# Optimization experiments

Measured on AMD Instinct MI355X. Metric: run time of the kernel, lower is better.

The kernel has to match this reference:

```python
import jax, jax.numpy as jnp
import numpy as np

B, N, E, G, V = 8, 512, 8192, 1024, 100000
HD, FIN, BN_EPS = 1024, 20, 1e-5


def setup_inputs() -> dict:
    key = jax.random.key(0)
    ks = jax.random.split(key, 8)
    return {
        'h': jax.random.normal(ks[0], (B, N, FIN), jnp.float32),
        'src': jax.random.randint(ks[1], (B, E), 0, N, jnp.int32),
        'dst': jax.random.randint(ks[2], (B, E), 0, N, jnp.int32),
        'gPos': jax.random.randint(ks[3], (B, G), 0, V, jnp.int32),
        'allDBGEmb': jax.random.normal(ks[4], (V, HD), jnp.float32),
        'fc_init_w': jax.random.normal(ks[5], (HD, FIN), jnp.float32) * (1.0 / np.sqrt(FIN)),
        'fc_init_b': jnp.zeros((HD,), jnp.float32),
        'bn1_g': jnp.ones((HD,), jnp.float32),
        'bn1_b': jnp.zeros((HD,), jnp.float32),
        'bn2_g': jnp.ones((HD,), jnp.float32),
        'bn2_b': jnp.zeros((HD,), jnp.float32),
        'fc_w': jax.random.normal(ks[6], (128, 2 * HD), jnp.float32) * (1.0 / np.sqrt(2 * HD)),
        'fc_b': jnp.zeros((128,), jnp.float32),
        'bn3_g': jnp.ones((128,), jnp.float32),
        'bn3_b': jnp.zeros((128,), jnp.float32),
        'fc2_w': jax.random.normal(ks[7], (1, 128), jnp.float32) * (1.0 / np.sqrt(128)),
        'fc2_b': jnp.zeros((1,), jnp.float32),
    }


def _bn(x, g, b):
    # BatchNorm1d in training mode: batch statistics over axis 0 (biased var)
    mu = x.mean(0)
    var = ((x - mu) ** 2).mean(0)
    return (x - mu) * jax.lax.rsqrt(var + BN_EPS) * g + b


def _gin_mean(x, s, d):
    # GINConv(None, 'mean') with eps=0: h_v + mean_{u in N(v)} h_u
    sums = jax.ops.segment_sum(x[s], d, num_segments=N)  # [N, HD]
    deg = jax.ops.segment_sum(jnp.ones((E, 1), x.dtype), d, num_segments=N)
    return x + jnp.where(deg > 0, sums / jnp.maximum(deg, 1.0), 0.0)


def reference(h, src, dst, gPos, allDBGEmb, fc_init_w, fc_init_b,
              bn1_g, bn1_b, bn2_g, bn2_b, fc_w, fc_b, bn3_g, bn3_b,
              fc2_w, fc2_b):
    def per_graph(hq, s, d, gp):
        x = hq @ fc_init_w.T + fc_init_b                      # [N, HD]
        x = jax.nn.relu(_bn(_gin_mean(x, s, d), bn1_g, bn1_b))
        x = jax.nn.relu(_bn(_gin_mean(x, s, d), bn2_g, bn2_b))
        qemb = x.mean(0)                                      # dgl.mean_nodes
        gEmb = allDBGEmb[gp]                                  # [G, HD]
        H = jnp.concatenate([jnp.broadcast_to(qemb, (G, HD)), gEmb], axis=1)
        h2 = jax.nn.relu(_bn(H @ fc_w.T + fc_b, bn3_g, bn3_b))
        return jax.nn.sigmoid(h2 @ fc2_w.T + fc2_b).reshape(-1)  # [G]

    return jax.vmap(per_graph)(h, src, dst, gPos)  # [B, G]
```

## Files before the change

### kernel.cpp

```cpp
#include <hip/hip_runtime.h>
#include <hip/hip_bf16.h>

#define B_ 8
#define G_ 1024
#define HD_ 1024
#define EPS_ 1e-5f


typedef __attribute__((ext_vector_type(8))) short bf16x8;
typedef __attribute__((ext_vector_type(4))) float f32x4;

__device__ inline short bf1(float x) {
    return (short)__builtin_bit_cast(unsigned short, __float2bfloat16(x));
}
__device__ inline bf16x8 cvt8(float4 a, float4 b) {
    bf16x8 o;
    o[0] = bf1(a.x); o[1] = bf1(a.y); o[2] = bf1(a.z); o[3] = bf1(a.w);
    o[4] = bf1(b.x); o[5] = bf1(b.y); o[6] = bf1(b.z); o[7] = bf1(b.w);
    return o;
}

__global__ __launch_bounds__(256) void k_w2cvt(const float* __restrict__ fc_w,
                                               short* __restrict__ w2arr) {
    int gid = blockIdx.x * 256 + threadIdx.x;
    int kt = gid >> 9;
    int jblk = (gid >> 6) & 7;
    int lane = gid & 63;
    int j = jblk * 16 + (lane & 15);
    int k = kt * 32 + (lane >> 4) * 8;
    const float4* sp = (const float4*)&fc_w[(size_t)j * (2 * HD_) + HD_ + k];
    *(bf16x8*)&w2arr[(size_t)gid * 8] = cvt8(sp[0], sp[1]);
}

#define ASLAB 258

__global__ __launch_bounds__(512) void k_gemm(const int* __restrict__ gPos,
                                              const float* __restrict__ emb,
                                              const short* __restrict__ w2arr,
                                              float* __restrict__ z,
                                              float* __restrict__ ps,
                                              float* __restrict__ pq) {
    int b = blockIdx.y, gblk = blockIdx.x;
    int gbase = gblk * 32;
    int tid = threadIdx.x;
    int wave = tid >> 6, lane = tid & 63;
    int gq = wave >> 2, jq = wave & 3;
    int l15 = lane & 15, kb = lane >> 4;

    __shared__ int gidx[32];
    __shared__ short As[2][16 * ASLAB];

    if (tid < 32) gidx[tid] = gPos[b * G_ + gbase + tid];
    __syncthreads();

    int arow = tid >> 4, acp = tid & 15;
    const float* abase = emb + (size_t)gidx[arow] * HD_;

    f32x4 acc0 = {0.f, 0.f, 0.f, 0.f}, acc1 = {0.f, 0.f, 0.f, 0.f};

    {
        const float4* ap = (const float4*)(abase + acp * 8);
        *(bf16x8*)&As[0][acp * ASLAB + arow * 8] = cvt8(ap[0], ap[1]);
    }
    __syncthreads();

    for (int p = 0; p < 8; ++p) {
        int cur = p & 1;
        if (p < 7) {
            const float4* ap = (const float4*)(abase + (p + 1) * 128 + acp * 8);
            *(bf16x8*)&As[cur ^ 1][acp * ASLAB + arow * 8] = cvt8(ap[0], ap[1]);
        }
#pragma unroll
        for (int kt = 0; kt < 4; ++kt) {
            bf16x8 a = *(const bf16x8*)&As[cur][(kt * 4 + kb) * ASLAB + (gq * 16 + l15) * 8];
            int f = (p * 4 + kt) * 8 + jq * 2;
            bf16x8 b0 = *(const bf16x8*)&w2arr[((size_t)f * 64 + lane) * 8];
            bf16x8 b1 = *(const bf16x8*)&w2arr[((size_t)(f + 1) * 64 + lane) * 8];
            acc0 = __builtin_amdgcn_mfma_f32_16x16x32_bf16(a, b0, acc0, 0, 0, 0);
            acc1 = __builtin_amdgcn_mfma_f32_16x16x32_bf16(a, b1, acc1, 0, 0, 0);
        }
        __syncthreads();
    }

    int col0 = jq * 32 + l15, col1 = col0 + 16;
    float s0 = 0.f, q0 = 0.f, s1 = 0.f, q1 = 0.f;
#pragma unroll
    for (int r = 0; r < 4; ++r) {
        int g = gbase + gq * 16 + kb * 4 + r;
        float z0 = acc0[r], z1 = acc1[r];
        z[(size_t)(b * G_ + g) * 128 + col0] = z0;
        z[(size_t)(b * G_ + g) * 128 + col1] = z1;
        s0 += z0; q0 += z0 * z0;
        s1 += z1; q1 += z1 * z1;
    }
    s0 += __shfl_xor(s0, 16, 64); s0 += __shfl_xor(s0, 32, 64);
    q0 += __shfl_xor(q0, 16, 64); q0 += __shfl_xor(q0, 32, 64);
    s1 += __shfl_xor(s1, 16, 64); s1 += __shfl_xor(s1, 32, 64);
    q1 += __shfl_xor(q1, 16, 64); q1 += __shfl_xor(q1, 32, 64);
    if (lane < 16) {
        int slot = (b * 64 + gblk * 2 + gq) * 128;
        ps[slot + col0] = s0; pq[slot + col0] = q0;
        ps[slot + col1] = s1; pq[slot + col1] = q1;
    }
}

__global__ void k_stats(const float* __restrict__ ps, const float* __restrict__ pq,
                        const float* __restrict__ g3, const float* __restrict__ b3,
                        float* __restrict__ scv, float* __restrict__ shv) {
    int b = blockIdx.x, j = threadIdx.x;
    float s = 0.f, q = 0.f;
#pragma unroll 8
    for (int t = 0; t < 64; ++t) {
        s += ps[(b * 64 + t) * 128 + j];
        q += pq[(b * 64 + t) * 128 + j];
    }
    float mu = s * (1.f / G_);
    float var = q * (1.f / G_) - mu * mu;
    float sc = g3[j] * rsqrtf(var + EPS_);
    scv[b * 128 + j] = sc;
    shv[b * 128 + j] = b3[j] - mu * sc;
}

__global__ __launch_bounds__(256) void k_final(const float* __restrict__ z,
                                               const float* __restrict__ scv,
                                               const float* __restrict__ shv,
                                               const float* __restrict__ fc2w,
                                               const float* __restrict__ fc2b,
                                               float* __restrict__ out) {
    int wid = (blockIdx.x * blockDim.x + threadIdx.x) >> 6;
    int lane = threadIdx.x & 63;
    int b = wid >> 10;
    const float* zr = z + (size_t)wid * 128;
    float acc = 0.f;
#pragma unroll
    for (int t = 0; t < 2; ++t) {
        int j = lane + t * 64;
        float v = fmaf(zr[j], scv[b * 128 + j], shv[b * 128 + j]);
        v = fmaxf(v, 0.f);
        acc += v * fc2w[j];
    }
    for (int off = 32; off; off >>= 1) acc += __shfl_down(acc, off, 64);
    if (lane == 0) out[wid] = 1.f / (1.f + expf(-(acc + fc2b[0])));
}

extern "C" void kernel_launch(void* const* d_in, const int* in_sizes, int n_in,
                              void* d_out, int out_size, void* d_ws, size_t ws_size,
                              hipStream_t stream) {
    const int*   gPos = (const int*)d_in[3];
    const float* emb  = (const float*)d_in[4];
    const float* fc_w = (const float*)d_in[11];
    const float* bn3g = (const float*)d_in[13];
    const float* bn3b = (const float*)d_in[14];
    const float* fc2w = (const float*)d_in[15];
    const float* fc2b = (const float*)d_in[16];
    float* out = (float*)d_out;

    char* w = (char*)d_ws;
    float* z     = (float*)w; w += (size_t)B_ * G_ * 128 * 4;
    short* w2arr = (short*)w; w += (size_t)128 * HD_ * 2;
    float* ps    = (float*)w; w += (size_t)B_ * 64 * 128 * 4;
    float* pq    = (float*)w; w += (size_t)B_ * 64 * 128 * 4;
    float* scv   = (float*)w; w += (size_t)B_ * 128 * 4;
    float* shv   = (float*)w; w += (size_t)B_ * 128 * 4;

    k_w2cvt<<<64, 256, 0, stream>>>(fc_w, w2arr);
    k_gemm<<<dim3(32, B_), 512, 0, stream>>>(gPos, emb, w2arr, z, ps, pq);
    k_stats<<<B_, 128, 0, stream>>>(ps, pq, bn3g, bn3b, scv, shv);
    k_final<<<(B_ * G_) / 4, 256, 0, stream>>>(z, scv, shv, fc2w, fc2b, out);
}
```

Baseline: 28.97 us.

## Fuse BN stats into final kernel, store z as bf16, load full A tile upfront

The separate stats kernel is removed, and each final block now recomputes the per-batch BN scale and shift from the partial sums before applying them. The intermediate z is stored as bf16 to halve its write and read traffic. The GEMM now gathers the whole 32x1024 embedding slab into LDS in one pass instead of a double-buffered loop, and each wave owns 16 columns and reuses one B fragment across two MFMAs. This saves a launch and some synchronisation, at the cost of redundant stats work per block, a larger LDS footprint and extra bf16 rounding on z before BN.

```diff
diff --git a/kernel.cpp b/kernel.cpp
--- a/kernel.cpp
+++ b/kernel.cpp
@@ -19,6 +19,9 @@
     o[4] = bf1(b.x); o[5] = bf1(b.y); o[6] = bf1(b.z); o[7] = bf1(b.w);
     return o;
 }
+__device__ inline float bf2f(unsigned short u) {
+    return __builtin_bit_cast(float, (unsigned)u << 16);
+}
 
 __global__ __launch_bounds__(256) void k_w2cvt(const float* __restrict__ fc_w,
                                                short* __restrict__ w2arr) {
@@ -32,115 +35,110 @@
     *(bf16x8*)&w2arr[(size_t)gid * 8] = cvt8(sp[0], sp[1]);
 }
 
-#define ASLAB 258
+#define SLABW 258
 
 __global__ __launch_bounds__(512) void k_gemm(const int* __restrict__ gPos,
                                               const float* __restrict__ emb,
                                               const short* __restrict__ w2arr,
-                                              float* __restrict__ z,
+                                              short* __restrict__ zb,
                                               float* __restrict__ ps,
                                               float* __restrict__ pq) {
     int b = blockIdx.y, gblk = blockIdx.x;
     int gbase = gblk * 32;
     int tid = threadIdx.x;
-    int wave = tid >> 6, lane = tid & 63;
-    int gq = wave >> 2, jq = wave & 3;
+    int jq = tid >> 6, lane = tid & 63;
     int l15 = lane & 15, kb = lane >> 4;
 
-    __shared__ int gidx[32];
-    __shared__ short As[2][16 * ASLAB];
-
-    if (tid < 32) gidx[tid] = gPos[b * G_ + gbase + tid];
-    __syncthreads();
-
-    int arow = tid >> 4, acp = tid & 15;
-    const float* abase = emb + (size_t)gidx[arow] * HD_;
-
-    f32x4 acc0 = {0.f, 0.f, 0.f, 0.f}, acc1 = {0.f, 0.f, 0.f, 0.f};
+    __shared__ short As[128 * SLABW];
 
     {
-        const float4* ap = (const float4*)(abase + acp * 8);
-        *(bf16x8*)&As[0][acp * ASLAB + arow * 8] = cvt8(ap[0], ap[1]);
+        int arow = tid >> 4, acp = tid & 15;
+        const float* abase = emb + (size_t)gPos[b * G_ + gbase + arow] * HD_;
+#pragma unroll
+        for (int i = 0; i < 8; ++i) {
+            int k = i * 128 + acp * 8;
+            const float4* ap = (const float4*)(abase + k);
+            *(bf16x8*)&As[(i * 16 + acp) * SLABW + arow * 8] = cvt8(ap[0], ap[1]);
+        }
     }
     __syncthreads();
 
-    for (int p = 0; p < 8; ++p) {
-        int cur = p & 1;
-        if (p < 7) {
-            const float4* ap = (const float4*)(abase + (p + 1) * 128 + acp * 8);
-            *(bf16x8*)&As[cur ^ 1][acp * ASLAB + arow * 8] = cvt8(ap[0], ap[1]);
-        }
-#pragma unroll
-        for (int kt = 0; kt < 4; ++kt) {
-            bf16x8 a = *(const bf16x8*)&As[cur][(kt * 4 + kb) * ASLAB + (gq * 16 + l15) * 8];
-            int f = (p * 4 + kt) * 8 + jq * 2;
-            bf16x8 b0 = *(const bf16x8*)&w2arr[((size_t)f * 64 + lane) * 8];
-            bf16x8 b1 = *(const bf16x8*)&w2arr[((size_t)(f + 1) * 64 + lane) * 8];
-            acc0 = __builtin_amdgcn_mfma_f32_16x16x32_bf16(a, b0, acc0, 0, 0, 0);
-            acc1 = __builtin_amdgcn_mfma_f32_16x16x32_bf16(a, b1, acc1, 0, 0, 0);
-        }
-        __syncthreads();
+    f32x4 acc0 = {0.f, 0.f, 0.f, 0.f}, acc1 = {0.f, 0.f, 0.f, 0.f};
+#pragma unroll 4
+    for (int kt = 0; kt < 32; ++kt) {
+        int f = kt * 8 + jq;
+        bf16x8 bv = *(const bf16x8*)&w2arr[((size_t)f * 64 + lane) * 8];
+        bf16x8 a0 = *(const bf16x8*)&As[(kt * 4 + kb) * SLABW + l15 * 8];
+        bf16x8 a1 = *(const bf16x8*)&As[(kt * 4 + kb) * SLABW + (16 + l15) * 8];
+        acc0 = __builtin_amdgcn_mfma_f32_16x16x32_bf16(a0, bv, acc0, 0, 0, 0);
+        acc1 = __builtin_amdgcn_mfma_f32_16x16x32_bf16(a1, bv, acc1, 0, 0, 0);
     }
 
-    int col0 = jq * 32 + l15, col1 = col0 + 16;
-    float s0 = 0.f, q0 = 0.f, s1 = 0.f, q1 = 0.f;
+    int jcol = jq * 16 + l15;
+    float s = 0.f, q = 0.f;
 #pragma unroll
     for (int r = 0; r < 4; ++r) {
-        int g = gbase + gq * 16 + kb * 4 + r;
-        float z0 = acc0[r], z1 = acc1[r];
-        z[(size_t)(b * G_ + g) * 128 + col0] = z0;
-        z[(size_t)(b * G_ + g) * 128 + col1] = z1;
-        s0 += z0; q0 += z0 * z0;
-        s1 += z1; q1 += z1 * z1;
+        float v0 = acc0[r], v1 = acc1[r];
+        int g0 = gbase + kb * 4 + r;
+        int g1 = g0 + 16;
+        zb[(size_t)(b * G_ + g0) * 128 + jcol] = bf1(v0);
+        zb[(size_t)(b * G_ + g1) * 128 + jcol] = bf1(v1);
+        s += v0 + v1;
+        q += v0 * v0 + v1 * v1;
     }
-    s0 += __shfl_xor(s0, 16, 64); s0 += __shfl_xor(s0, 32, 64);
-    q0 += __shfl_xor(q0, 16, 64); q0 += __shfl_xor(q0, 32, 64);
-    s1 += __shfl_xor(s1, 16, 64); s1 += __shfl_xor(s1, 32, 64);
-    q1 += __shfl_xor(q1, 16, 64); q1 += __shfl_xor(q1, 32, 64);
+    s += __shfl_xor(s, 16, 64); s += __shfl_xor(s, 32, 64);
+    q += __shfl_xor(q, 16, 64); q += __shfl_xor(q, 32, 64);
     if (lane < 16) {
-        int slot = (b * 64 + gblk * 2 + gq) * 128;
-        ps[slot + col0] = s0; pq[slot + col0] = q0;
-        ps[slot + col1] = s1; pq[slot + col1] = q1;
+        ps[(b * 32 + gblk) * 128 + jcol] = s;
+        pq[(b * 32 + gblk) * 128 + jcol] = q;
     }
 }
 
-__global__ void k_stats(const float* __restrict__ ps, const float* __restrict__ pq,
-                        const float* __restrict__ g3, const float* __restrict__ b3,
-                        float* __restrict__ scv, float* __restrict__ shv) {
-    int b = blockIdx.x, j = threadIdx.x;
-    float s = 0.f, q = 0.f;
-#pragma unroll 8
-    for (int t = 0; t < 64; ++t) {
-        s += ps[(b * 64 + t) * 128 + j];
-        q += pq[(b * 64 + t) * 128 + j];
-    }
-    float mu = s * (1.f / G_);
-    float var = q * (1.f / G_) - mu * mu;
-    float sc = g3[j] * rsqrtf(var + EPS_);
-    scv[b * 128 + j] = sc;
-    shv[b * 128 + j] = b3[j] - mu * sc;
-}
-
-__global__ __launch_bounds__(256) void k_final(const float* __restrict__ z,
-                                               const float* __restrict__ scv,
-                                               const float* __restrict__ shv,
+__global__ __launch_bounds__(256) void k_final(const short* __restrict__ zb,
+                                               const float* __restrict__ ps,
+                                               const float* __restrict__ pq,
+                                               const float* __restrict__ g3,
+                                               const float* __restrict__ b3,
                                                const float* __restrict__ fc2w,
                                                const float* __restrict__ fc2b,
                                                float* __restrict__ out) {
-    int wid = (blockIdx.x * blockDim.x + threadIdx.x) >> 6;
-    int lane = threadIdx.x & 63;
-    int b = wid >> 10;
-    const float* zr = z + (size_t)wid * 128;
-    float acc = 0.f;
+    int b = blockIdx.y, gseg = blockIdx.x;
+    int tid = threadIdx.x, wave = tid >> 6, lane = tid & 63;
+    __shared__ float scL[128], shL[128];
+    if (tid < 128) {
+        int j = tid;
+        float s = 0.f, q = 0.f;
+#pragma unroll 8
+        for (int t = 0; t < 32; ++t) {
+            s += ps[(b * 32 + t) * 128 + j];
+            q += pq[(b * 32 + t) * 128 + j];
+        }
+        float mu = s * (1.f / G_);
+        float var = q * (1.f / G_) - mu * mu;
+        float sc = g3[j] * rsqrtf(var + EPS_);
+        scL[j] = sc;
+        shL[j] = b3[j] - mu * sc;
+    }
+    __syncthreads();
+    int j0 = lane * 2;
+    float sc0 = scL[j0], sc1 = scL[j0 + 1];
+    float sh0 = shL[j0], sh1 = shL[j0 + 1];
+    float w0 = fc2w[j0], w1 = fc2w[j0 + 1], bias = fc2b[0];
 #pragma unroll
-    for (int t = 0; t < 2; ++t) {
-        int j = lane + t * 64;
-        float v = fmaf(zr[j], scv[b * 128 + j], shv[b * 128 + j]);
-        v = fmaxf(v, 0.f);
-        acc += v * fc2w[j];
+    for (int it = 0; it < 16; ++it) {
+        int g = gseg * 64 + it * 4 + wave;
+        const ushort2* zr = (const ushort2*)(zb + (size_t)(b * G_ + g) * 128);
+        ushort2 u = zr[lane];
+        float acc = fmaxf(fmaf(bf2f(u.x), sc0, sh0), 0.f) * w0 +
+                    fmaxf(fmaf(bf2f(u.y), sc1, sh1), 0.f) * w1;
+        acc += __shfl_xor(acc, 32, 64);
+        acc += __shfl_xor(acc, 16, 64);
+        acc += __shfl_xor(acc, 8, 64);
+        acc += __shfl_xor(acc, 4, 64);
+        acc += __shfl_xor(acc, 2, 64);
+        acc += __shfl_xor(acc, 1, 64);
+        if (lane == 0) out[b * G_ + g] = 1.f / (1.f + expf(-(acc + bias)));
     }
-    for (int off = 32; off; off >>= 1) acc += __shfl_down(acc, off, 64);
-    if (lane == 0) out[wid] = 1.f / (1.f + expf(-(acc + fc2b[0])));
 }
 
 extern "C" void kernel_launch(void* const* d_in, const int* in_sizes, int n_in,
@@ -156,15 +154,12 @@
     float* out = (float*)d_out;
 
     char* w = (char*)d_ws;
-    float* z     = (float*)w; w += (size_t)B_ * G_ * 128 * 4;
+    short* zb    = (short*)w; w += (size_t)B_ * G_ * 128 * 2;
     short* w2arr = (short*)w; w += (size_t)128 * HD_ * 2;
-    float* ps    = (float*)w; w += (size_t)B_ * 64 * 128 * 4;
-    float* pq    = (float*)w; w += (size_t)B_ * 64 * 128 * 4;
-    float* scv   = (float*)w; w += (size_t)B_ * 128 * 4;
-    float* shv   = (float*)w; w += (size_t)B_ * 128 * 4;
+    float* ps    = (float*)w; w += (size_t)B_ * 32 * 128 * 4;
+    float* pq    = (float*)w; w += (size_t)B_ * 32 * 128 * 4;
 
     k_w2cvt<<<64, 256, 0, stream>>>(fc_w, w2arr);
-    k_gemm<<<dim3(32, B_), 512, 0, stream>>>(gPos, emb, w2arr, z, ps, pq);
-    k_stats<<<B_, 128, 0, stream>>>(ps, pq, bn3g, bn3b, scv, shv);
-    k_final<<<(B_ * G_) / 4, 256, 0, stream>>>(z, scv, shv, fc2w, fc2b, out);
+    k_gemm<<<dim3(32, B_), 512, 0, stream>>>(gPos, emb, w2arr, zb, ps, pq);
+    k_final<<<dim3(16, B_), 256, 0, stream>>>(zb, ps, pq, bn3g, bn3b, fc2w, fc2b, out);
 }
```

New measurement: 31.07 us. 7.3% more time.

## Fuse BN stats and final head into GEMM kernel via per-batch grid barrier

Applied to the files above, without the earlier changes.

Merges the stats and final kernels into the GEMM kernel. The last-arriving block per batch, detected with an atomic counter, reduces the partial sums and publishes scale and shift, and the other blocks spin-wait on a flag before applying BN, ReLU, fc2 and sigmoid straight from the MFMA accumulators. This drops the z intermediate round-trip and two kernel launches. The K loop also now stages 256 columns per step (4 iterations instead of 8), which halves the barriers. The spin-wait assumes all 256 blocks are co-resident, otherwise it can deadlock.

```diff
diff --git a/kernel.cpp b/kernel.cpp
--- a/kernel.cpp
+++ b/kernel.cpp
@@ -5,6 +5,7 @@
 #define G_ 1024
 #define HD_ 1024
 #define EPS_ 1e-5f
+#define AGENT_ __HIP_MEMORY_SCOPE_AGENT
 
 
 typedef __attribute__((ext_vector_type(8))) short bf16x8;
@@ -21,8 +22,10 @@
 }
 
 __global__ __launch_bounds__(256) void k_w2cvt(const float* __restrict__ fc_w,
-                                               short* __restrict__ w2arr) {
+                                               short* __restrict__ w2arr,
+                                               int* __restrict__ sync_) {
     int gid = blockIdx.x * 256 + threadIdx.x;
+    if (blockIdx.x == 0 && threadIdx.x < 16) sync_[threadIdx.x] = 0;
     int kt = gid >> 9;
     int jblk = (gid >> 6) & 7;
     int lane = gid & 63;
@@ -32,14 +35,21 @@
     *(bf16x8*)&w2arr[(size_t)gid * 8] = cvt8(sp[0], sp[1]);
 }
 
-#define ASLAB 258
+#define SLABW 258
 
 __global__ __launch_bounds__(512) void k_gemm(const int* __restrict__ gPos,
                                               const float* __restrict__ emb,
                                               const short* __restrict__ w2arr,
-                                              float* __restrict__ z,
+                                              const float* __restrict__ g3,
+                                              const float* __restrict__ b3,
+                                              const float* __restrict__ fc2w,
+                                              const float* __restrict__ fc2b,
                                               float* __restrict__ ps,
-                                              float* __restrict__ pq) {
+                                              float* __restrict__ pq,
+                                              float* __restrict__ scv,
+                                              float* __restrict__ shv,
+                                              int* __restrict__ sync_,
+                                              float* __restrict__ out) {
     int b = blockIdx.y, gblk = blockIdx.x;
     int gbase = gblk * 32;
     int tid = threadIdx.x;
@@ -47,35 +57,38 @@
     int gq = wave >> 2, jq = wave & 3;
     int l15 = lane & 15, kb = lane >> 4;
 
-    __shared__ int gidx[32];
-    __shared__ short As[2][16 * ASLAB];
-
-    if (tid < 32) gidx[tid] = gPos[b * G_ + gbase + tid];
-    __syncthreads();
+    __shared__ short As[2][32 * SLABW];
+    __shared__ float sp4[4][128], sq4[4][128];
+    __shared__ float wred[4][32];
+    __shared__ int lastflag;
 
     int arow = tid >> 4, acp = tid & 15;
-    const float* abase = emb + (size_t)gidx[arow] * HD_;
+    const float* abase = emb + (size_t)gPos[b * G_ + gbase + arow] * HD_;
+
+    {
+        const float4* a0 = (const float4*)(abase + acp * 8);
+        const float4* a1 = (const float4*)(abase + (acp + 16) * 8);
+        *(bf16x8*)&As[0][acp * SLABW + arow * 8] = cvt8(a0[0], a0[1]);
+        *(bf16x8*)&As[0][(acp + 16) * SLABW + arow * 8] = cvt8(a1[0], a1[1]);
+    }
+    __syncthreads();
 
     f32x4 acc0 = {0.f, 0.f, 0.f, 0.f}, acc1 = {0.f, 0.f, 0.f, 0.f};
-
-    {
-        const float4* ap = (const float4*)(abase + acp * 8);
-        *(bf16x8*)&As[0][acp * ASLAB + arow * 8] = cvt8(ap[0], ap[1]);
-    }
-    __syncthreads();
-
-    for (int p = 0; p < 8; ++p) {
+    for (int p = 0; p < 4; ++p) {
         int cur = p & 1;
-        if (p < 7) {
-            const float4* ap = (const float4*)(abase + (p + 1) * 128 + acp * 8);
-            *(bf16x8*)&As[cur ^ 1][acp * ASLAB + arow * 8] = cvt8(ap[0], ap[1]);
+        if (p < 3) {
+            const float* ab = abase + (p + 1) * 256;
+            const float4* a0 = (const float4*)(ab + acp * 8);
+            const float4* a1 = (const float4*)(ab + (acp + 16) * 8);
+            *(bf16x8*)&As[cur ^ 1][acp * SLABW + arow * 8] = cvt8(a0[0], a0[1]);
+            *(bf16x8*)&As[cur ^ 1][(acp + 16) * SLABW + arow * 8] = cvt8(a1[0], a1[1]);
         }
 #pragma unroll
-        for (int kt = 0; kt < 4; ++kt) {
-            bf16x8 a = *(const bf16x8*)&As[cur][(kt * 4 + kb) * ASLAB + (gq * 16 + l15) * 8];
-            int f = (p * 4 + kt) * 8 + jq * 2;
+        for (int kt = 0; kt < 8; ++kt) {
+            int f = (p * 8 + kt) * 8 + jq * 2;
             bf16x8 b0 = *(const bf16x8*)&w2arr[((size_t)f * 64 + lane) * 8];
             bf16x8 b1 = *(const bf16x8*)&w2arr[((size_t)(f + 1) * 64 + lane) * 8];
+            bf16x8 a = *(const bf16x8*)&As[cur][(kt * 4 + kb) * SLABW + (gq * 16 + l15) * 8];
             acc0 = __builtin_amdgcn_mfma_f32_16x16x32_bf16(a, b0, acc0, 0, 0, 0);
             acc1 = __builtin_amdgcn_mfma_f32_16x16x32_bf16(a, b1, acc1, 0, 0, 0);
         }
@@ -83,64 +96,83 @@
     }
 
     int col0 = jq * 32 + l15, col1 = col0 + 16;
-    float s0 = 0.f, q0 = 0.f, s1 = 0.f, q1 = 0.f;
+    {
+        float s0 = 0.f, q0 = 0.f, s1 = 0.f, q1 = 0.f;
+#pragma unroll
+        for (int r = 0; r < 4; ++r) {
+            float v0 = acc0[r], v1 = acc1[r];
+            s0 += v0; q0 += v0 * v0;
+            s1 += v1; q1 += v1 * v1;
+        }
+        s0 += __shfl_xor(s0, 16, 64); s0 += __shfl_xor(s0, 32, 64);
+        q0 += __shfl_xor(q0, 16, 64); q0 += __shfl_xor(q0, 32, 64);
+        s1 += __shfl_xor(s1, 16, 64); s1 += __shfl_xor(s1, 32, 64);
+        q1 += __shfl_xor(q1, 16, 64); q1 += __shfl_xor(q1, 32, 64);
+        if (lane < 16) {
+            int slot = (b * 64 + gblk * 2 + gq) * 128;
+            __hip_atomic_store(&ps[slot + col0], s0, __ATOMIC_RELAXED, AGENT_);
+            __hip_atomic_store(&pq[slot + col0], q0, __ATOMIC_RELAXED, AGENT_);
+            __hip_atomic_store(&ps[slot + col1], s1, __ATOMIC_RELAXED, AGENT_);
+            __hip_atomic_store(&pq[slot + col1], q1, __ATOMIC_RELAXED, AGENT_);
+        }
+    }
+    __syncthreads();
+    if (tid == 0) {
+        int old = __hip_atomic_fetch_add(&sync_[b], 1, __ATOMIC_ACQ_REL, AGENT_);
+        lastflag = (old == 31);
+    }
+    __syncthreads();
+
+    if (lastflag) {
+        int sgrp = tid >> 7, j = tid & 127;
+        float ss = 0.f, qq = 0.f;
+        for (int t = sgrp; t < 64; t += 4) {
+            ss += __hip_atomic_load(&ps[(b * 64 + t) * 128 + j], __ATOMIC_RELAXED, AGENT_);
+            qq += __hip_atomic_load(&pq[(b * 64 + t) * 128 + j], __ATOMIC_RELAXED, AGENT_);
+        }
+        sp4[sgrp][j] = ss;
+        sq4[sgrp][j] = qq;
+        __syncthreads();
+        if (tid < 128) {
+            float S = sp4[0][tid] + sp4[1][tid] + sp4[2][tid] + sp4[3][tid];
+            float Q = sq4[0][tid] + sq4[1][tid] + sq4[2][tid] + sq4[3][tid];
+            float mu = S * (1.f / G_);
+            float var = Q * (1.f / G_) - mu * mu;
+            float sc = g3[tid] * rsqrtf(var + EPS_);
+            __hip_atomic_store(&scv[b * 128 + tid], sc, __ATOMIC_RELAXED, AGENT_);
+            __hip_atomic_store(&shv[b * 128 + tid], b3[tid] - mu * sc,
+                               __ATOMIC_RELAXED, AGENT_);
+        }
+        __syncthreads();
+        if (tid == 0)
+            __hip_atomic_store(&sync_[8 + b], 1, __ATOMIC_RELEASE, AGENT_);
+    }
+
+    if (tid == 0) {
+        while (__hip_atomic_load(&sync_[8 + b], __ATOMIC_ACQUIRE, AGENT_) == 0) {}
+    }
+    __syncthreads();
+
+    float sc0 = __hip_atomic_load(&scv[b * 128 + col0], __ATOMIC_RELAXED, AGENT_);
+    float sc1 = __hip_atomic_load(&scv[b * 128 + col1], __ATOMIC_RELAXED, AGENT_);
+    float sh0 = __hip_atomic_load(&shv[b * 128 + col0], __ATOMIC_RELAXED, AGENT_);
+    float sh1 = __hip_atomic_load(&shv[b * 128 + col1], __ATOMIC_RELAXED, AGENT_);
+    float w0 = fc2w[col0], w1 = fc2w[col1];
 #pragma unroll
     for (int r = 0; r < 4; ++r) {
-        int g = gbase + gq * 16 + kb * 4 + r;
-        float z0 = acc0[r], z1 = acc1[r];
-        z[(size_t)(b * G_ + g) * 128 + col0] = z0;
-        z[(size_t)(b * G_ + g) * 128 + col1] = z1;
-        s0 += z0; q0 += z0 * z0;
-        s1 += z1; q1 += z1 * z1;
-    }
-    s0 += __shfl_xor(s0, 16, 64); s0 += __shfl_xor(s0, 32, 64);
-    q0 += __shfl_xor(q0, 16, 64); q0 += __shfl_xor(q0, 32, 64);
-    s1 += __shfl_xor(s1, 16, 64); s1 += __shfl_xor(s1, 32, 64);
-    q1 += __shfl_xor(q1, 16, 64); q1 += __shfl_xor(q1, 32, 64);
-    if (lane < 16) {
-        int slot = (b * 64 + gblk * 2 + gq) * 128;
-        ps[slot + col0] = s0; pq[slot + col0] = q0;
-        ps[slot + col1] = s1; pq[slot + col1] = q1;
-    }
-}
-
-__global__ void k_stats(const float* __restrict__ ps, const float* __restrict__ pq,
-                        const float* __restrict__ g3, const float* __restrict__ b3,
-                        float* __restrict__ scv, float* __restrict__ shv) {
-    int b = blockIdx.x, j = threadIdx.x;
-    float s = 0.f, q = 0.f;
-#pragma unroll 8
-    for (int t = 0; t < 64; ++t) {
-        s += ps[(b * 64 + t) * 128 + j];
-        q += pq[(b * 64 + t) * 128 + j];
-    }
-    float mu = s * (1.f / G_);
-    float var = q * (1.f / G_) - mu * mu;
-    float sc = g3[j] * rsqrtf(var + EPS_);
-    scv[b * 128 + j] = sc;
-    shv[b * 128 + j] = b3[j] - mu * sc;
-}
-
-__global__ __launch_bounds__(256) void k_final(const float* __restrict__ z,
-                                               const float* __restrict__ scv,
-                                               const float* __restrict__ shv,
-                                               const float* __restrict__ fc2w,
-                                               const float* __restrict__ fc2b,
-                                               float* __restrict__ out) {
-    int wid = (blockIdx.x * blockDim.x + threadIdx.x) >> 6;
-    int lane = threadIdx.x & 63;
-    int b = wid >> 10;
-    const float* zr = z + (size_t)wid * 128;
-    float acc = 0.f;
-#pragma unroll
-    for (int t = 0; t < 2; ++t) {
-        int j = lane + t * 64;
-        float v = fmaf(zr[j], scv[b * 128 + j], shv[b * 128 + j]);
-        v = fmaxf(v, 0.f);
-        acc += v * fc2w[j];
-    }
-    for (int off = 32; off; off >>= 1) acc += __shfl_down(acc, off, 64);
-    if (lane == 0) out[wid] = 1.f / (1.f + expf(-(acc + fc2b[0])));
+        float t = fmaxf(fmaf(acc0[r], sc0, sh0), 0.f) * w0 +
+                  fmaxf(fmaf(acc1[r], sc1, sh1), 0.f) * w1;
+        t += __shfl_xor(t, 1, 64);
+        t += __shfl_xor(t, 2, 64);
+        t += __shfl_xor(t, 4, 64);
+        t += __shfl_xor(t, 8, 64);
+        if (l15 == 0) wred[jq][gq * 16 + kb * 4 + r] = t;
+    }
+    __syncthreads();
+    if (tid < 32) {
+        float tot = wred[0][tid] + wred[1][tid] + wred[2][tid] + wred[3][tid] + fc2b[0];
+        out[b * G_ + gbase + tid] = 1.f / (1.f + expf(-tot));
+    }
 }
 
 extern "C" void kernel_launch(void* const* d_in, const int* in_sizes, int n_in,
@@ -156,15 +188,14 @@
     float* out = (float*)d_out;
 
     char* w = (char*)d_ws;
-    float* z     = (float*)w; w += (size_t)B_ * G_ * 128 * 4;
     short* w2arr = (short*)w; w += (size_t)128 * HD_ * 2;
     float* ps    = (float*)w; w += (size_t)B_ * 64 * 128 * 4;
     float* pq    = (float*)w; w += (size_t)B_ * 64 * 128 * 4;
     float* scv   = (float*)w; w += (size_t)B_ * 128 * 4;
     float* shv   = (float*)w; w += (size_t)B_ * 128 * 4;
-
-    k_w2cvt<<<64, 256, 0, stream>>>(fc_w, w2arr);
-    k_gemm<<<dim3(32, B_), 512, 0, stream>>>(gPos, emb, w2arr, z, ps, pq);
-    k_stats<<<B_, 128, 0, stream>>>(ps, pq, bn3g, bn3b, scv, shv);
-    k_final<<<(B_ * G_) / 4, 256, 0, stream>>>(z, scv, shv, fc2w, fc2b, out);
-}
+    int*   sync_ = (int*)w;   w += 64;
+
+    k_w2cvt<<<64, 256, 0, stream>>>(fc_w, w2arr, sync_);
+    k_gemm<<<dim3(32, B_), 512, 0, stream>>>(gPos, emb, w2arr, bn3g, bn3b,
+                                             fc2w, fc2b, ps, pq, scv, shv, sync_, out);
+}
```

After: 56.50 us. 1.95x slower.

## Fuse BN stats into final kernel and store GEMM output as bf16

Applied to the files above, without the earlier changes.

Removes the separate k_stats launch: each k_final block recomputes the per-batch BN scale and shift from the partial sums into shared memory. The intermediate z is stored as bf16 rather than fp32, halving its write and read traffic. k_final is regridded so each wave handles 16 rows with a full xor reduction. The cost is redundant stat computation across 16 blocks per batch and bf16 rounding of z before normalization, while the statistics themselves stay in fp32.

```diff
diff --git a/kernel.cpp b/kernel.cpp
--- a/kernel.cpp
+++ b/kernel.cpp
@@ -19,6 +19,9 @@
     o[4] = bf1(b.x); o[5] = bf1(b.y); o[6] = bf1(b.z); o[7] = bf1(b.w);
     return o;
 }
+__device__ inline float bf2f(unsigned short u) {
+    return __builtin_bit_cast(float, (unsigned)u << 16);
+}
 
 __global__ __launch_bounds__(256) void k_w2cvt(const float* __restrict__ fc_w,
                                                short* __restrict__ w2arr) {
@@ -37,7 +40,7 @@
 __global__ __launch_bounds__(512) void k_gemm(const int* __restrict__ gPos,
                                               const float* __restrict__ emb,
                                               const short* __restrict__ w2arr,
-                                              float* __restrict__ z,
+                                              short* __restrict__ zb,
                                               float* __restrict__ ps,
                                               float* __restrict__ pq) {
     int b = blockIdx.y, gblk = blockIdx.x;
@@ -88,8 +91,8 @@
     for (int r = 0; r < 4; ++r) {
         int g = gbase + gq * 16 + kb * 4 + r;
         float z0 = acc0[r], z1 = acc1[r];
-        z[(size_t)(b * G_ + g) * 128 + col0] = z0;
-        z[(size_t)(b * G_ + g) * 128 + col1] = z1;
+        zb[(size_t)(b * G_ + g) * 128 + col0] = bf1(z0);
+        zb[(size_t)(b * G_ + g) * 128 + col1] = bf1(z1);
         s0 += z0; q0 += z0 * z0;
         s1 += z1; q1 += z1 * z1;
     }
@@ -104,43 +107,51 @@
     }
 }
 
-__global__ void k_stats(const float* __restrict__ ps, const float* __restrict__ pq,
-                        const float* __restrict__ g3, const float* __restrict__ b3,
-                        float* __restrict__ scv, float* __restrict__ shv) {
-    int b = blockIdx.x, j = threadIdx.x;
-    float s = 0.f, q = 0.f;
-#pragma unroll 8
-    for (int t = 0; t < 64; ++t) {
-        s += ps[(b * 64 + t) * 128 + j];
-        q += pq[(b * 64 + t) * 128 + j];
-    }
-    float mu = s * (1.f / G_);
-    float var = q * (1.f / G_) - mu * mu;
-    float sc = g3[j] * rsqrtf(var + EPS_);
-    scv[b * 128 + j] = sc;
-    shv[b * 128 + j] = b3[j] - mu * sc;
-}
-
-__global__ __launch_bounds__(256) void k_final(const float* __restrict__ z,
-                                               const float* __restrict__ scv,
-                                               const float* __restrict__ shv,
+__global__ __launch_bounds__(256) void k_final(const short* __restrict__ zb,
+                                               const float* __restrict__ ps,
+                                               const float* __restrict__ pq,
+                                               const float* __restrict__ g3,
+                                               const float* __restrict__ b3,
                                                const float* __restrict__ fc2w,
                                                const float* __restrict__ fc2b,
                                                float* __restrict__ out) {
-    int wid = (blockIdx.x * blockDim.x + threadIdx.x) >> 6;
-    int lane = threadIdx.x & 63;
-    int b = wid >> 10;
-    const float* zr = z + (size_t)wid * 128;
-    float acc = 0.f;
+    int b = blockIdx.y, gseg = blockIdx.x;
+    int tid = threadIdx.x, wave = tid >> 6, lane = tid & 63;
+    __shared__ float scL[128], shL[128];
+    if (tid < 128) {
+        int j = tid;
+        float s = 0.f, q = 0.f;
+#pragma unroll 8
+        for (int t = 0; t < 64; ++t) {
+            s += ps[(b * 64 + t) * 128 + j];
+            q += pq[(b * 64 + t) * 128 + j];
+        }
+        float mu = s * (1.f / G_);
+        float var = q * (1.f / G_) - mu * mu;
+        float sc = g3[j] * rsqrtf(var + EPS_);
+        scL[j] = sc;
+        shL[j] = b3[j] - mu * sc;
+    }
+    __syncthreads();
+    int j0 = lane * 2;
+    float sc0 = scL[j0], sc1 = scL[j0 + 1];
+    float sh0 = shL[j0], sh1 = shL[j0 + 1];
+    float w0 = fc2w[j0], w1 = fc2w[j0 + 1], bias = fc2b[0];
 #pragma unroll
-    for (int t = 0; t < 2; ++t) {
-        int j = lane + t * 64;
-        float v = fmaf(zr[j], scv[b * 128 + j], shv[b * 128 + j]);
-        v = fmaxf(v, 0.f);
-        acc += v * fc2w[j];
+    for (int it = 0; it < 16; ++it) {
+        int g = gseg * 64 + it * 4 + wave;
+        const ushort2* zr = (const ushort2*)(zb + (size_t)(b * G_ + g) * 128);
+        ushort2 u = zr[lane];
+        float acc = fmaxf(fmaf(bf2f(u.x), sc0, sh0), 0.f) * w0 +
+                    fmaxf(fmaf(bf2f(u.y), sc1, sh1), 0.f) * w1;
+        acc += __shfl_xor(acc, 32, 64);
+        acc += __shfl_xor(acc, 16, 64);
+        acc += __shfl_xor(acc, 8, 64);
+        acc += __shfl_xor(acc, 4, 64);
+        acc += __shfl_xor(acc, 2, 64);
+        acc += __shfl_xor(acc, 1, 64);
+        if (lane == 0) out[b * G_ + g] = 1.f / (1.f + expf(-(acc + bias)));
     }
-    for (int off = 32; off; off >>= 1) acc += __shfl_down(acc, off, 64);
-    if (lane == 0) out[wid] = 1.f / (1.f + expf(-(acc + fc2b[0])));
 }
 
 extern "C" void kernel_launch(void* const* d_in, const int* in_sizes, int n_in,
@@ -156,15 +167,12 @@
     float* out = (float*)d_out;
 
     char* w = (char*)d_ws;
-    float* z     = (float*)w; w += (size_t)B_ * G_ * 128 * 4;
+    short* zb    = (short*)w; w += (size_t)B_ * G_ * 128 * 2;
     short* w2arr = (short*)w; w += (size_t)128 * HD_ * 2;
     float* ps    = (float*)w; w += (size_t)B_ * 64 * 128 * 4;
     float* pq    = (float*)w; w += (size_t)B_ * 64 * 128 * 4;
-    float* scv   = (float*)w; w += (size_t)B_ * 128 * 4;
-    float* shv   = (float*)w; w += (size_t)B_ * 128 * 4;
 
     k_w2cvt<<<64, 256, 0, stream>>>(fc_w, w2arr);
-    k_gemm<<<dim3(32, B_), 512, 0, stream>>>(gPos, emb, w2arr, z, ps, pq);
-    k_stats<<<B_, 128, 0, stream>>>(ps, pq, bn3g, bn3b, scv, shv);
-    k_final<<<(B_ * G_) / 4, 256, 0, stream>>>(z, scv, shv, fc2w, fc2b, out);
+    k_gemm<<<dim3(32, B_), 512, 0, stream>>>(gPos, emb, w2arr, zb, ps, pq);
+    k_final<<<dim3(16, B_), 256, 0, stream>>>(zb, ps, pq, bn3g, bn3b, fc2w, fc2b, out);
 }
```

Result: slower. 34.20 us (+18.1%).
